# Kernel tuning notes

Measured on AMD Instinct MI355X. Metric: run time of the kernel, lower is better.

## Reference

```python
import jax, jax.numpy as jnp
import numpy as np


def setup_inputs() -> dict:
    key = jax.random.key(0)
    k1, k2, k3, k4 = jax.random.split(key, 4)
    b, l, v, s = 2, 2048, 8, 64
    return {
        "query": jax.random.normal(k1, (b, l, v, s), dtype=jnp.float32),
        "key": jax.random.normal(k2, (b, l, v, s), dtype=jnp.float32),
        "value": jax.random.normal(k3, (b, l, v, s), dtype=jnp.float32),
        "label_arr": jax.random.randint(k4, (b, l), 0, 8, dtype=jnp.int64),
    }


def reference(query, key, value, label_arr):
    # query/key/value: (b, l, v, s); label_arr computed into a mask in the
    # original code but never applied, so it does not affect the math.
    b, l, v, s = query.shape
    scale = 1.0 / np.sqrt(s).astype(np.float32)
    # key summed over the v (head) axis -> pooled key per token: (b, l, s)
    sum_tot_vec = key.sum(axis=2)
    # scores[b,l,v,m] = <query[b,l,v,:], sum_tot_vec[b,m,:]>  (the torch per-v loop, batched)
    scores = jnp.einsum("blvs,bms->blvm", query, sum_tot_vec)
    A = jax.nn.softmax(scale * scores, axis=-1)  # (b, l, v, l)
    # V[b,l,v,s] = sum_m A[b,l,v,m] * value[b,m,v,s]  (the broadcast-multiply+sum, as a matmul)
    V = jnp.einsum("blvm,bmvs->blvs", A, value)
    return V
```

## Files before the change

### kernel.cpp

```cpp
#include <hip/hip_runtime.h>


#define BB 2
#define LL 2048
#define HH 8
#define DD 64

typedef __attribute__((ext_vector_type(8)))  short  short8;
typedef __attribute__((ext_vector_type(16))) float  float16v;

static __device__ inline unsigned short f2bf(float x) {
    union { float f; unsigned u; } v; v.f = x;
    unsigned r = v.u + 0x7FFF + ((v.u >> 16) & 1);
    return (unsigned short)(r >> 16);
}
static __device__ inline unsigned pk_bf2(float x, float y) {
    return (unsigned)f2bf(x) | ((unsigned)f2bf(y) << 16);
}

__global__ __launch_bounds__(256)
void prep_kernel(const float* __restrict__ key, const float* __restrict__ value,
                 unsigned short* __restrict__ kswz,
                 unsigned short* __restrict__ vswz) {
    __shared__ __align__(16) float Vl[64][68];
    int bid = blockIdx.x;
    int tid = threadIdx.x;

    if (bid < 512) {
        int mt = bid & 31, bh = bid >> 5;
        int h = bh & 7, b = bh >> 3;
        int m0 = mt * 64;
#pragma unroll
        for (int k = 0; k < 4; ++k) {
            int f = tid + k * 256;
            int r = f >> 4;
            int cc = (f & 15) * 4;
            float4 t = *(const float4*)(value +
                (((size_t)(b * LL + m0 + r)) * HH + h) * DD + cc);
            *(float4*)&Vl[r][cc] = t;
        }
        __syncthreads();
#pragma unroll
        for (int k = 0; k < 2; ++k) {
            int c    = tid + k * 256;
            int Tl   = c >> 8;
            int t    = (c >> 7) & 1;
            int vh   = (c >> 6) & 1;
            int lane = c & 63;
            int ln = lane & 31, half = lane >> 5;
            union { short8 v; unsigned short u[8]; } o;
#pragma unroll
            for (int jj = 0; jj < 8; ++jj) {
                int r2 = t * 8 + jj;
                int m  = (r2 & 3) + 8 * (r2 >> 2) + 4 * half;
                o.u[jj] = f2bf(Vl[Tl * 32 + m][vh * 32 + ln]);
            }
            *(short8*)(vswz +
                ((((size_t)bh * 64 + (mt * 2 + Tl)) * 4 + t * 2 + vh) * 512)
                + lane * 8) = o.v;
        }
    } else {
        const float LOG2E = 1.4426950408889634f;
        int pb    = bid - 512;
        int chunk = pb * 4 + (tid >> 6);
        int lane  = tid & 63;
        int b = chunk >> 8, T = (chunk >> 2) & 63, ks = chunk & 3;
        int ln = lane & 31, hf = lane >> 5;
        const float* base = key + (((size_t)(b * LL + T * 32 + ln)) * HH) * DD
                                + ks * 16 + hf * 8;
        float s[8];
#pragma unroll
        for (int j = 0; j < 8; ++j) s[j] = 0.f;
#pragma unroll
        for (int v = 0; v < HH; ++v) {
            float4 f0 = *(const float4*)(base + v * DD);
            float4 f1 = *(const float4*)(base + v * DD + 4);
            s[0] += f0.x; s[1] += f0.y; s[2] += f0.z; s[3] += f0.w;
            s[4] += f1.x; s[5] += f1.y; s[6] += f1.z; s[7] += f1.w;
        }
        union { short8 v; unsigned u[4]; } o;
#pragma unroll
        for (int i = 0; i < 4; ++i)
            o.u[i] = pk_bf2(s[2 * i] * LOG2E, s[2 * i + 1] * LOG2E);
        *(short8*)(kswz + (size_t)chunk * 512 + lane * 8) = o.v;
    }
}

__global__ __launch_bounds__(256, 2)
void attn_kernel(const float* __restrict__ query,
                 const unsigned short* __restrict__ kswz,
                 const unsigned short* __restrict__ vswz,
                 float* __restrict__ out) {
    int bid = blockIdx.x;
    int bh  = bid & 15;
    int qt  = bid >> 4;
    int h = bh & 7, b = bh >> 3;

    int tid  = threadIdx.x;
    int lane = tid & 63;
    int wv   = tid >> 6;
    int ln   = lane & 31;
    int half = lane >> 5;

    __shared__ float O2[2][64][68];
    __shared__ float lsumL[4][128];
    __shared__ float invL[64];

    short8 qf[2][4];
#pragma unroll
    for (int g = 0; g < 2; ++g) {
        const float* qbase = query +
            (((size_t)(b * LL + qt * 64 + g * 32 + ln)) * HH + h) * DD;
#pragma unroll
        for (int ks = 0; ks < 4; ++ks) {
            const float4* qp = (const float4*)(qbase + ks * 16 + half * 8);
            float4 t0 = qp[0], t1 = qp[1];
            union { short8 v; unsigned u[4]; } uq;
            uq.u[0] = pk_bf2(t0.x * 0.125f, t0.y * 0.125f);
            uq.u[1] = pk_bf2(t0.z * 0.125f, t0.w * 0.125f);
            uq.u[2] = pk_bf2(t1.x * 0.125f, t1.y * 0.125f);
            uq.u[3] = pk_bf2(t1.z * 0.125f, t1.w * 0.125f);
            qf[g][ks] = uq.v;
        }
    }

    const unsigned short* kp0 = kswz + (((size_t)b * 64 + wv * 16) * 4) * 512
                                     + (size_t)lane * 8;
    const unsigned short* vp0 = vswz + (((size_t)bh * 64 + wv * 16) * 4) * 512
                                     + (size_t)lane * 8;

    float16v o00, o01, o10, o11;
#pragma unroll
    for (int i = 0; i < 16; ++i) { o00[i] = 0.f; o01[i] = 0.f; o10[i] = 0.f; o11[i] = 0.f; }
    float ls0a = 0.f, ls0b = 0.f, ls1a = 0.f, ls1b = 0.f;

    short8 kf[4], vf[4];
#pragma unroll
    for (int ks = 0; ks < 4; ++ks) kf[ks] = *(const short8*)(kp0 + ks * 512);
#pragma unroll
    for (int u = 0; u < 4; ++u)    vf[u]  = *(const short8*)(vp0 + u * 512);

#pragma unroll
    for (int it = 0; it < 16; ++it) {
        float16v s0, s1;
#pragma unroll
        for (int i = 0; i < 16; ++i) { s0[i] = 0.f; s1[i] = 0.f; }
#pragma unroll
        for (int ks = 0; ks < 4; ++ks) {
            s0 = __builtin_amdgcn_mfma_f32_32x32x16_bf16(kf[ks], qf[0][ks], s0, 0, 0, 0);
            s1 = __builtin_amdgcn_mfma_f32_32x32x16_bf16(kf[ks], qf[1][ks], s1, 0, 0, 0);
        }
        if (it + 1 < 16) {
#pragma unroll
            for (int ks = 0; ks < 4; ++ks)
                kf[ks] = *(const short8*)(kp0 + (it + 1) * 2048 + ks * 512);
        }

        union { short8 v[2]; unsigned u[8]; } pu0, pu1;
#pragma unroll
        for (int i = 0; i < 8; ++i) {
            union { float f; unsigned u; } e0, e1;
            e0.f = exp2f(s0[2 * i]);
            e1.f = exp2f(s0[2 * i + 1]);
            ls0a += e0.f; ls0b += e1.f;
            pu0.u[i] = __builtin_amdgcn_perm(e1.u + 0x8000u, e0.u + 0x8000u, 0x07060302u);
        }
#pragma unroll
        for (int i = 0; i < 8; ++i) {
            union { float f; unsigned u; } e0, e1;
            e0.f = exp2f(s1[2 * i]);
            e1.f = exp2f(s1[2 * i + 1]);
            ls1a += e0.f; ls1b += e1.f;
            pu1.u[i] = __builtin_amdgcn_perm(e1.u + 0x8000u, e0.u + 0x8000u, 0x07060302u);
        }

        o00 = __builtin_amdgcn_mfma_f32_32x32x16_bf16(pu0.v[0], vf[0], o00, 0, 0, 0);
        o01 = __builtin_amdgcn_mfma_f32_32x32x16_bf16(pu0.v[0], vf[1], o01, 0, 0, 0);
        o10 = __builtin_amdgcn_mfma_f32_32x32x16_bf16(pu1.v[0], vf[0], o10, 0, 0, 0);
        o11 = __builtin_amdgcn_mfma_f32_32x32x16_bf16(pu1.v[0], vf[1], o11, 0, 0, 0);
        o00 = __builtin_amdgcn_mfma_f32_32x32x16_bf16(pu0.v[1], vf[2], o00, 0, 0, 0);
        o01 = __builtin_amdgcn_mfma_f32_32x32x16_bf16(pu0.v[1], vf[3], o01, 0, 0, 0);
        o10 = __builtin_amdgcn_mfma_f32_32x32x16_bf16(pu1.v[1], vf[2], o10, 0, 0, 0);
        o11 = __builtin_amdgcn_mfma_f32_32x32x16_bf16(pu1.v[1], vf[3], o11, 0, 0, 0);

        if (it + 1 < 16) {
#pragma unroll
            for (int u = 0; u < 4; ++u)
                vf[u] = *(const short8*)(vp0 + (it + 1) * 2048 + u * 512);
        }
    }

    lsumL[wv][lane]      = ls0a + ls0b;
    lsumL[wv][64 + lane] = ls1a + ls1b;
    if (wv < 2) {
#pragma unroll
        for (int r = 0; r < 16; ++r) {
            int row = (r & 3) + 8 * (r >> 2) + 4 * half;
            O2[wv][row][ln]           = o00[r];
            O2[wv][row][32 + ln]      = o01[r];
            O2[wv][32 + row][ln]      = o10[r];
            O2[wv][32 + row][32 + ln] = o11[r];
        }
    }
    __syncthreads();
    if (wv >= 2) {
#pragma unroll
        for (int r = 0; r < 16; ++r) {
            int row = (r & 3) + 8 * (r >> 2) + 4 * half;
            O2[wv - 2][row][ln]           += o00[r];
            O2[wv - 2][row][32 + ln]      += o01[r];
            O2[wv - 2][32 + row][ln]      += o10[r];
            O2[wv - 2][32 + row][32 + ln] += o11[r];
        }
    }
    __syncthreads();

    if (tid < 64) {
        int g = tid >> 5, c = tid & 31;
        float s = 0.f;
#pragma unroll
        for (int w = 0; w < 4; ++w)
            s += lsumL[w][g * 64 + c] + lsumL[w][g * 64 + 32 + c];
        invL[tid] = 1.0f / s;
    }
    __syncthreads();

    int qrow = tid >> 2;
    int c16  = (tid & 3) * 16;
    float inv = invL[qrow];
    float buf[16];
#pragma unroll
    for (int j = 0; j < 16; ++j)
        buf[j] = (O2[0][qrow][c16 + j] + O2[1][qrow][c16 + j]) * inv;
    float* ob = out + (((size_t)(b * LL + qt * 64 + qrow)) * HH + h) * DD + c16;
#pragma unroll
    for (int j = 0; j < 4; ++j)
        *(float4*)(ob + 4 * j) = make_float4(buf[4 * j], buf[4 * j + 1],
                                             buf[4 * j + 2], buf[4 * j + 3]);
}

extern "C" void kernel_launch(void* const* d_in, const int* in_sizes, int n_in,
                              void* d_out, int out_size, void* d_ws, size_t ws_size,
                              hipStream_t stream) {
    const float* query = (const float*)d_in[0];
    const float* key   = (const float*)d_in[1];
    const float* value = (const float*)d_in[2];
    float* out = (float*)d_out;

    unsigned short* kswz = (unsigned short*)d_ws;
    unsigned short* vswz = (unsigned short*)((char*)d_ws + 512 * 1024);

    prep_kernel<<<640, 256, 0, stream>>>(key, value, kswz, vswz);
    attn_kernel<<<512, 256, 0, stream>>>(query, kswz, vswz, out);
}
```

Before: 106.2 us.

## Use 512-thread blocks covering 128 query rows and switch to hardware exp2

Each attention block now has 8 waves and covers 128 query rows instead of 64. Pairs of waves share the same key/value slices, so K/V loads can be reused in cache across two query halves. The grid shrinks to 256 blocks. The epilogue reduces the two query halves one after the other through the same shared buffer, which adds barriers. Separately, exp2f is replaced by the raw amdgcn exp2 builtin to skip range handling. Fewer blocks than CUs (256) may leave some compute units idle.

```diff
diff --git a/kernel.cpp b/kernel.cpp
--- a/kernel.cpp
+++ b/kernel.cpp
@@ -16,6 +16,13 @@
 }
 static __device__ inline unsigned pk_bf2(float x, float y) {
     return (unsigned)f2bf(x) | ((unsigned)f2bf(y) << 16);
+}
+static __device__ inline float fast_exp2(float x) {
+#if __has_builtin(__builtin_amdgcn_exp2f)
+    return __builtin_amdgcn_exp2f(x);
+#else
+    return exp2f(x);
+#endif
 }
 
 __global__ __launch_bounds__(256)
@@ -86,7 +93,7 @@
     }
 }
 
-__global__ __launch_bounds__(256, 2)
+__global__ __launch_bounds__(512, 2)
 void attn_kernel(const float* __restrict__ query,
                  const unsigned short* __restrict__ kswz,
                  const unsigned short* __restrict__ vswz,
@@ -99,18 +106,20 @@
     int tid  = threadIdx.x;
     int lane = tid & 63;
     int wv   = tid >> 6;
+    int qh   = wv & 1;
+    int kh   = wv >> 1;
     int ln   = lane & 31;
     int half = lane >> 5;
 
     __shared__ float O2[2][64][68];
-    __shared__ float lsumL[4][128];
-    __shared__ float invL[64];
+    __shared__ float lsumL[8][128];
+    __shared__ float invL[128];
 
     short8 qf[2][4];
 #pragma unroll
     for (int g = 0; g < 2; ++g) {
         const float* qbase = query +
-            (((size_t)(b * LL + qt * 64 + g * 32 + ln)) * HH + h) * DD;
+            (((size_t)(b * LL + qt * 128 + qh * 64 + g * 32 + ln)) * HH + h) * DD;
 #pragma unroll
         for (int ks = 0; ks < 4; ++ks) {
             const float4* qp = (const float4*)(qbase + ks * 16 + half * 8);
@@ -124,9 +133,9 @@
         }
     }
 
-    const unsigned short* kp0 = kswz + (((size_t)b * 64 + wv * 16) * 4) * 512
+    const unsigned short* kp0 = kswz + (((size_t)b * 64 + kh * 16) * 4) * 512
                                      + (size_t)lane * 8;
-    const unsigned short* vp0 = vswz + (((size_t)bh * 64 + wv * 16) * 4) * 512
+    const unsigned short* vp0 = vswz + (((size_t)bh * 64 + kh * 16) * 4) * 512
                                      + (size_t)lane * 8;
 
     float16v o00, o01, o10, o11;
@@ -160,16 +169,16 @@
 #pragma unroll
         for (int i = 0; i < 8; ++i) {
             union { float f; unsigned u; } e0, e1;
-            e0.f = exp2f(s0[2 * i]);
-            e1.f = exp2f(s0[2 * i + 1]);
+            e0.f = fast_exp2(s0[2 * i]);
+            e1.f = fast_exp2(s0[2 * i + 1]);
             ls0a += e0.f; ls0b += e1.f;
             pu0.u[i] = __builtin_amdgcn_perm(e1.u + 0x8000u, e0.u + 0x8000u, 0x07060302u);
         }
 #pragma unroll
         for (int i = 0; i < 8; ++i) {
             union { float f; unsigned u; } e0, e1;
-            e0.f = exp2f(s1[2 * i]);
-            e1.f = exp2f(s1[2 * i + 1]);
+            e0.f = fast_exp2(s1[2 * i]);
+            e1.f = fast_exp2(s1[2 * i + 1]);
             ls1a += e0.f; ls1b += e1.f;
             pu1.u[i] = __builtin_amdgcn_perm(e1.u + 0x8000u, e0.u + 0x8000u, 0x07060302u);
         }
@@ -192,51 +201,96 @@
 
     lsumL[wv][lane]      = ls0a + ls0b;
     lsumL[wv][64 + lane] = ls1a + ls1b;
-    if (wv < 2) {
+
+    if (qh == 0 && kh < 2) {
 #pragma unroll
         for (int r = 0; r < 16; ++r) {
             int row = (r & 3) + 8 * (r >> 2) + 4 * half;
-            O2[wv][row][ln]           = o00[r];
-            O2[wv][row][32 + ln]      = o01[r];
-            O2[wv][32 + row][ln]      = o10[r];
-            O2[wv][32 + row][32 + ln] = o11[r];
-        }
-    }
-    __syncthreads();
-    if (wv >= 2) {
+            O2[kh][row][ln]           = o00[r];
+            O2[kh][row][32 + ln]      = o01[r];
+            O2[kh][32 + row][ln]      = o10[r];
+            O2[kh][32 + row][32 + ln] = o11[r];
+        }
+    }
+    __syncthreads();
+
+    if (tid < 128) {
+        int qhh = tid >> 6, g = (tid >> 5) & 1, c = tid & 31;
+        float s = 0.f;
+#pragma unroll
+        for (int k4 = 0; k4 < 4; ++k4) {
+            int w = 2 * k4 + qhh;
+            s += lsumL[w][g * 64 + c] + lsumL[w][g * 64 + 32 + c];
+        }
+        invL[tid] = 1.0f / s;
+    }
+    if (qh == 0 && kh >= 2) {
 #pragma unroll
         for (int r = 0; r < 16; ++r) {
             int row = (r & 3) + 8 * (r >> 2) + 4 * half;
-            O2[wv - 2][row][ln]           += o00[r];
-            O2[wv - 2][row][32 + ln]      += o01[r];
-            O2[wv - 2][32 + row][ln]      += o10[r];
-            O2[wv - 2][32 + row][32 + ln] += o11[r];
-        }
-    }
-    __syncthreads();
-
-    if (tid < 64) {
-        int g = tid >> 5, c = tid & 31;
-        float s = 0.f;
-#pragma unroll
-        for (int w = 0; w < 4; ++w)
-            s += lsumL[w][g * 64 + c] + lsumL[w][g * 64 + 32 + c];
-        invL[tid] = 1.0f / s;
-    }
-    __syncthreads();
-
-    int qrow = tid >> 2;
-    int c16  = (tid & 3) * 16;
-    float inv = invL[qrow];
-    float buf[16];
-#pragma unroll
-    for (int j = 0; j < 16; ++j)
-        buf[j] = (O2[0][qrow][c16 + j] + O2[1][qrow][c16 + j]) * inv;
-    float* ob = out + (((size_t)(b * LL + qt * 64 + qrow)) * HH + h) * DD + c16;
-#pragma unroll
-    for (int j = 0; j < 4; ++j)
-        *(float4*)(ob + 4 * j) = make_float4(buf[4 * j], buf[4 * j + 1],
-                                             buf[4 * j + 2], buf[4 * j + 3]);
+            O2[kh - 2][row][ln]           += o00[r];
+            O2[kh - 2][row][32 + ln]      += o01[r];
+            O2[kh - 2][32 + row][ln]      += o10[r];
+            O2[kh - 2][32 + row][32 + ln] += o11[r];
+        }
+    }
+    __syncthreads();
+
+    {
+        int R = tid >> 3, c8 = (tid & 7) * 8;
+        float inv = invL[R];
+        float* ob = out + (((size_t)(b * LL + qt * 128 + R)) * HH + h) * DD + c8;
+        float4 r0, r1;
+        r0.x = (O2[0][R][c8 + 0] + O2[1][R][c8 + 0]) * inv;
+        r0.y = (O2[0][R][c8 + 1] + O2[1][R][c8 + 1]) * inv;
+        r0.z = (O2[0][R][c8 + 2] + O2[1][R][c8 + 2]) * inv;
+        r0.w = (O2[0][R][c8 + 3] + O2[1][R][c8 + 3]) * inv;
+        r1.x = (O2[0][R][c8 + 4] + O2[1][R][c8 + 4]) * inv;
+        r1.y = (O2[0][R][c8 + 5] + O2[1][R][c8 + 5]) * inv;
+        r1.z = (O2[0][R][c8 + 6] + O2[1][R][c8 + 6]) * inv;
+        r1.w = (O2[0][R][c8 + 7] + O2[1][R][c8 + 7]) * inv;
+        *(float4*)ob = r0; *(float4*)(ob + 4) = r1;
+    }
+    __syncthreads();
+
+    if (qh == 1 && kh < 2) {
+#pragma unroll
+        for (int r = 0; r < 16; ++r) {
+            int row = (r & 3) + 8 * (r >> 2) + 4 * half;
+            O2[kh][row][ln]           = o00[r];
+            O2[kh][row][32 + ln]      = o01[r];
+            O2[kh][32 + row][ln]      = o10[r];
+            O2[kh][32 + row][32 + ln] = o11[r];
+        }
+    }
+    __syncthreads();
+    if (qh == 1 && kh >= 2) {
+#pragma unroll
+        for (int r = 0; r < 16; ++r) {
+            int row = (r & 3) + 8 * (r >> 2) + 4 * half;
+            O2[kh - 2][row][ln]           += o00[r];
+            O2[kh - 2][row][32 + ln]      += o01[r];
+            O2[kh - 2][32 + row][ln]      += o10[r];
+            O2[kh - 2][32 + row][32 + ln] += o11[r];
+        }
+    }
+    __syncthreads();
+
+    {
+        int R = tid >> 3, c8 = (tid & 7) * 8;
+        float inv = invL[64 + R];
+        float* ob = out + (((size_t)(b * LL + qt * 128 + 64 + R)) * HH + h) * DD + c8;
+        float4 r0, r1;
+        r0.x = (O2[0][R][c8 + 0] + O2[1][R][c8 + 0]) * inv;
+        r0.y = (O2[0][R][c8 + 1] + O2[1][R][c8 + 1]) * inv;
+        r0.z = (O2[0][R][c8 + 2] + O2[1][R][c8 + 2]) * inv;
+        r0.w = (O2[0][R][c8 + 3] + O2[1][R][c8 + 3]) * inv;
+        r1.x = (O2[0][R][c8 + 4] + O2[1][R][c8 + 4]) * inv;
+        r1.y = (O2[0][R][c8 + 5] + O2[1][R][c8 + 5]) * inv;
+        r1.z = (O2[0][R][c8 + 6] + O2[1][R][c8 + 6]) * inv;
+        r1.w = (O2[0][R][c8 + 7] + O2[1][R][c8 + 7]) * inv;
+        *(float4*)ob = r0; *(float4*)(ob + 4) = r1;
+    }
 }
 
 extern "C" void kernel_launch(void* const* d_in, const int* in_sizes, int n_in,
@@ -251,5 +305,5 @@
     unsigned short* vswz = (unsigned short*)((char*)d_ws + 512 * 1024);
 
     prep_kernel<<<640, 256, 0, stream>>>(key, value, kswz, vswz);
-    attn_kernel<<<512, 256, 0, stream>>>(query, kswz, vswz, out);
-}
+    attn_kernel<<<256, 512, 0, stream>>>(query, kswz, vswz, out);
+}
```

Result: faster. 100.3 us (-5.6%).
